# Kernel tuning notes

Hardware: AMD Instinct MI355X
Metric: run time of the kernel (lower is better)

The kernel has to match this reference:

```python
import jax, jax.numpy as jnp
import numpy as np
from jax import lax

B, C, D, H, W = 2, 1, 128, 128, 128
CONSCIOUSNESS_WEIGHT = 0.1


def _field(depth, height, width, dtype):
    # sin(2*pi*(d+h+w)/(D+H+W)) broadcast over batch/channel
    d = jnp.arange(depth, dtype=dtype)[:, None, None]
    h = jnp.arange(height, dtype=dtype)[None, :, None]
    w = jnp.arange(width, dtype=dtype)[None, None, :]
    phase = 2.0 * jnp.pi * (d + h + w) / (depth + height + width)
    return jnp.sin(phase)  # [D,H,W]


def _conv3d(x, w, b):
    y = lax.conv_general_dilated(
        x, w, window_strides=(1, 1, 1), padding='SAME',
        dimension_numbers=('NCDHW', 'OIDHW', 'NCDHW'))
    return y + b[None, :, None, None, None]


def setup_inputs() -> dict:
    key = jax.random.key(0)
    ks = jax.random.split(key, 4)
    fan1 = 1 * 27
    fan2 = 8 * 27
    fan3 = 16 * 27
    return {
        'cube_data': jax.random.normal(ks[0], (B, C, D, H, W), dtype=jnp.float32),
        'w1': jax.random.normal(ks[1], (8, 1, 3, 3, 3), dtype=jnp.float32) / np.sqrt(fan1),
        'b1': jnp.zeros((8,), dtype=jnp.float32),
        'w2': jax.random.normal(ks[2], (16, 8, 3, 3, 3), dtype=jnp.float32) / np.sqrt(fan2),
        'b2': jnp.zeros((16,), dtype=jnp.float32),
        'w3': jax.random.normal(ks[3], (1, 16, 3, 3, 3), dtype=jnp.float32) / np.sqrt(fan3),
        'b3': jnp.zeros((1,), dtype=jnp.float32),
    }


def reference(cube_data, w1, b1, w2, b2, w3, b3):
    _, _, d, h, w = cube_data.shape
    field = _field(d, h, w, cube_data.dtype)[None, None]  # [1,1,D,H,W]
    integrated = cube_data * (1.0 + CONSCIOUSNESS_WEIGHT * field)
    x = jax.nn.relu(_conv3d(integrated, w1, b1))
    x = jax.nn.relu(_conv3d(x, w2, b2))
    x = jnp.tanh(_conv3d(x, w3, b3))
    return x
```

## Files before the change

kernel.cpp:

```cpp
#include <hip/hip_runtime.h>
#include <hip/hip_fp16.h>

#define VOX (128 * 128 * 128)
#define P 130
#define PP (P * P)
#define PVOX (P * P * P)
#define LROW 130
#define PLANE (6 * LROW)

typedef unsigned short u16;
typedef _Float16 f16x2 __attribute__((ext_vector_type(2)));
typedef _Float16 f16x8 __attribute__((ext_vector_type(8)));
typedef __attribute__((ext_vector_type(4))) float f32x4;

__device__ __forceinline__ u16 f2h(float f) {
    return __builtin_bit_cast(unsigned short, (_Float16)f);
}
__device__ __forceinline__ unsigned pkh_relu(float a, float b) {
    float ra = a > 0.f ? a : 0.f, rb = b > 0.f ? b : 0.f;
    return (unsigned)f2h(ra) | ((unsigned)f2h(rb) << 16);
}
__device__ __forceinline__ f16x2 h2(unsigned u) { return __builtin_bit_cast(f16x2, u); }

__device__ __forceinline__ float dot2(unsigned a, unsigned b, float c) {
#if __has_builtin(__builtin_amdgcn_fdot2)
    return __builtin_amdgcn_fdot2(h2(a), h2(b), c, false);
#else
    f16x2 av = h2(a), bv = h2(b);
    c = fmaf((float)av.x, (float)bv.x, c);
    return fmaf((float)av.y, (float)bv.y, c);
#endif
}

__device__ __forceinline__ float fast_tanh(float x) {
    float e = __expf(2.0f * x);
    return 1.0f - 2.0f * __builtin_amdgcn_rcpf(1.0f + e);
}

__device__ __forceinline__ void gload_lds16(const u16* g, u16* l) {
    __builtin_amdgcn_global_load_lds(
        (const __attribute__((address_space(1))) unsigned int*)g,
        (__attribute__((address_space(3))) unsigned int*)l,
        16, 0, 0);
}

__global__ __launch_bounds__(256) void integrate_kernel(
    const float* __restrict__ in, u16* __restrict__ x0,
    const float* __restrict__ w1, const float* __restrict__ w2,
    const float* __restrict__ w3, u16* __restrict__ w2frag,
    unsigned* __restrict__ w3p, float* __restrict__ w1c,
    u16* __restrict__ x1, u16* __restrict__ x2) {
    int i = blockIdx.x * 256 + threadIdx.x;
    if (i < 3584) {
        int j = i & 7, l = (i >> 3) & 63, s = i >> 9;
        int tap = s * 4 + (l >> 4), oc = l & 15;
        float v = (tap < 27) ? w2[(oc * 8 + j) * 27 + tap] : 0.0f;
        w2frag[i] = f2h(v);
    }
    if (i < 216) {
        int tap = i >> 3, j = i & 7;
        w3p[i] = (unsigned)f2h(w3[(2 * j) * 27 + tap]) |
                 ((unsigned)f2h(w3[(2 * j + 1) * 27 + tap]) << 16);
        int c = i & 7;
        w1c[i] = w1[c * 27 + tap];
    }
    if (i >= PVOX) return;
    int d = i / PP;
    int r = i - d * PP;
    int h = r / P;
    int w = r - h * P;
    const bool interior = (d >= 1 && d <= 128 && h >= 1 && h <= 128 && w >= 1 && w <= 128);
    float v = 0.0f;
    if (interior) {
        int s = (d - 1) + (h - 1) + (w - 1);
        float fld = 1.0f + 0.1f * __sinf(6.283185307179586f * (float)s / 384.0f);
        v = in[(size_t)(d - 1) * 16384 + (h - 1) * 128 + (w - 1)] * fld;
    } else {
        uint4 z = {0u, 0u, 0u, 0u};
        *(uint4*)(x1 + (size_t)i * 8) = z;
        *(uint4*)(x2 + (size_t)i * 16) = z;
        *(uint4*)(x2 + (size_t)i * 16 + 8) = z;
    }
    x0[i] = f2h(v);
}

__global__ __launch_bounds__(256) void integrate_light_kernel(
    const float* __restrict__ in, u16* __restrict__ x0) {
    const int i = blockIdx.x * 256 + threadIdx.x;
    const int d = i >> 14, h = (i >> 7) & 127, w = i & 127;
    const int s = d + h + w;
    const float fld = 1.0f + 0.1f * __sinf((float)s * 0.016362461737446838f);
    x0[(size_t)(d + 1) * PP + (h + 1) * P + (w + 1)] = f2h(in[i] * fld);
}

__global__ __launch_bounds__(256) void conv1_kernel(
    const u16* __restrict__ x0, const float* __restrict__ w1c,
    const float* __restrict__ b1, u16* __restrict__ x1) {
    const int t = blockIdx.x * 256 + threadIdx.x;
    const int w0 = (t & 63) * 2;
    const int h0 = ((t >> 6) & 31) * 4;
    const int d = t >> 11;

    float acc[4][2][8];
#pragma unroll
    for (int c = 0; c < 8; ++c) {
        const float b = b1[c];
#pragma unroll
        for (int i = 0; i < 4; ++i) { acc[i][0][c] = b; acc[i][1][c] = b; }
    }

#pragma unroll
    for (int dz = 0; dz < 3; ++dz) {
        const u16* zb = x0 + (size_t)(d + dz) * PP + (size_t)h0 * P + w0;
        const float* wz = w1c + dz * 9 * 8;
#pragma unroll
        for (int r = 0; r < 6; ++r) {
            const u16* rp = zb + r * P;
            const unsigned u0 = *(const unsigned*)rp;
            const unsigned u1 = *(const unsigned*)(rp + 2);
            float vv[4];
            vv[0] = (float)h2(u0).x; vv[1] = (float)h2(u0).y;
            vv[2] = (float)h2(u1).x; vv[3] = (float)h2(u1).y;
#pragma unroll
            for (int dy = 0; dy < 3; ++dy) {
                const int i = r - dy;
                if (i < 0 || i > 3) continue;
#pragma unroll
                for (int dx = 0; dx < 3; ++dx) {
                    const float a0 = vv[dx];
                    const float a1 = vv[dx + 1];
                    const float* wp = wz + (dy * 3 + dx) * 8;
#pragma unroll
                    for (int c = 0; c < 8; ++c) {
                        const float wt = wp[c];
                        acc[i][0][c] = fmaf(wt, a0, acc[i][0][c]);
                        acc[i][1][c] = fmaf(wt, a1, acc[i][1][c]);
                    }
                }
            }
        }
    }
    const size_t e0 = ((size_t)(d + 1) * P + (h0 + 1)) * P + (w0 + 1);
#pragma unroll
    for (int i = 0; i < 4; ++i) {
        uint4 oA, oB;
        oA.x = pkh_relu(acc[i][0][0], acc[i][0][1]);
        oA.y = pkh_relu(acc[i][0][2], acc[i][0][3]);
        oA.z = pkh_relu(acc[i][0][4], acc[i][0][5]);
        oA.w = pkh_relu(acc[i][0][6], acc[i][0][7]);
        oB.x = pkh_relu(acc[i][1][0], acc[i][1][1]);
        oB.y = pkh_relu(acc[i][1][2], acc[i][1][3]);
        oB.z = pkh_relu(acc[i][1][4], acc[i][1][5]);
        oB.w = pkh_relu(acc[i][1][6], acc[i][1][7]);
        *(uint4*)(x1 + (e0 + (size_t)i * P) * 8) = oA;
        *(uint4*)(x1 + (e0 + (size_t)i * P + 1) * 8) = oB;
    }
}

__global__ __launch_bounds__(256) void conv2_mfma_kernel(
    const u16* __restrict__ x1, const u16* __restrict__ w2frag,
    const float* __restrict__ b2, u16* __restrict__ x2) {
    __shared__ u16 sm[4 * PLANE * 8];

    const int tid = threadIdx.x;
    const int lane = tid & 63;
    const int wv = tid >> 6;
    const int q = lane >> 4;
    const int mi = lane & 15;
    const int D0 = (blockIdx.x >> 5) * 8;
    const int h0 = (blockIdx.x & 31) * 4;

    f16x8 wf[7];
#pragma unroll
    for (int s = 0; s < 7; ++s)
        wf[s] = *(const f16x8*)(w2frag + (size_t)(s * 64 + lane) * 8);

#pragma unroll
    for (int p = 0; p < 3; ++p) {
        const int pd = D0 + p;
        const int slot = pd & 3;
        const u16* gb = x1 + ((size_t)(pd * P + h0) * P) * 8;
        u16* lb = sm + (size_t)slot * PLANE * 8;
#pragma unroll
        for (int k = 0; k < 3; ++k) {
            const int u0 = wv * 64 + k * 256;
            gload_lds16(gb + (size_t)(u0 + lane) * 8, lb + (size_t)u0 * 8);
        }
        if (wv == 0 && lane < PLANE - 768)
            gload_lds16(gb + (size_t)(768 + lane) * 8, lb + (size_t)768 * 8);
    }
    __syncthreads();

    const float4 bv = *(const float4*)(b2 + q * 4);

#pragma unroll 1
    for (int i = 0; i < 8; ++i) {
        const int dout = D0 + i;

        if (i < 7) {
            const int pd = dout + 3;
            const int slot = pd & 3;
            const u16* gb = x1 + ((size_t)(pd * P + h0) * P) * 8;
            u16* lb = sm + (size_t)slot * PLANE * 8;
#pragma unroll
            for (int k = 0; k < 3; ++k) {
                const int u0 = wv * 64 + k * 256;
                gload_lds16(gb + (size_t)(u0 + lane) * 8, lb + (size_t)u0 * 8);
            }
            if (wv == 0 && lane < PLANE - 768)
                gload_lds16(gb + (size_t)(768 + lane) * 8, lb + (size_t)768 * 8);
        }

        f32x4 acc[8];
#pragma unroll
        for (int t = 0; t < 8; ++t) acc[t] = (f32x4){0.f, 0.f, 0.f, 0.f};

#pragma unroll
        for (int s = 0; s < 7; ++s) {
            int tap = s * 4 + q;
            if (tap > 26) tap = 26;
            const int dz = tap / 9;
            const int rem = tap - dz * 9;
            const int dy = rem / 3;
            const int dx = rem - dy * 3;
            const int slot = (dout + dz) & 3;
            const u16* bp = sm + ((size_t)(slot * 6 + wv + dy) * LROW + (mi + dx)) * 8;
#pragma unroll
            for (int t = 0; t < 8; ++t) {
                f16x8 act = *(const f16x8*)(bp + t * 128);
                acc[t] = __builtin_amdgcn_mfma_f32_16x16x32_f16(wf[s], act, acc[t], 0, 0, 0);
            }
        }

        const size_t obase = ((size_t)(dout + 1) * P + (h0 + wv + 1)) * P + 1;
#pragma unroll
        for (int t = 0; t < 8; ++t) {
            uint2 o;
            o.x = pkh_relu(acc[t][0] + bv.x, acc[t][1] + bv.y);
            o.y = pkh_relu(acc[t][2] + bv.z, acc[t][3] + bv.w);
            *(uint2*)(x2 + (obase + 16 * t + mi) * 16 + q * 4) = o;
        }

        if (i < 7) __syncthreads();
    }
}

__global__ __launch_bounds__(256) void conv3_kernel(
    const u16* __restrict__ x2, const unsigned* __restrict__ w3p,
    const float* __restrict__ b3, float* __restrict__ out) {
    const int t = blockIdx.x * 256 + threadIdx.x;
    const int w0 = (t & 63) * 2;
    const int h0 = ((t >> 6) & 31) * 4;
    const int d0 = (t >> 11) * 2;

    float accA[2][4][2], accB[2][4][2];
#pragma unroll
    for (int dd = 0; dd < 2; ++dd)
#pragma unroll
        for (int i = 0; i < 4; ++i)
#pragma unroll
            for (int m = 0; m < 2; ++m) { accA[dd][i][m] = 0.f; accB[dd][i][m] = 0.f; }

#pragma unroll 1
    for (int z = 0; z < 4; ++z) {
        const u16* zb = x2 + ((size_t)((d0 + z) * P + h0) * P + w0) * 16;
#pragma unroll
        for (int r = 0; r < 6; ++r) {
            const u16* rp = zb + (size_t)r * (P * 16);
            uint4 v[8];
#pragma unroll
            for (int k = 0; k < 8; ++k) v[k] = *(const uint4*)(rp + k * 8);
#pragma unroll
            for (int dd = 0; dd < 2; ++dd) {
                const int dz = z - dd;
                if (dz < 0 || dz > 2) continue;
                const unsigned* wz = w3p + dz * 9 * 8;
#pragma unroll
                for (int dy = 0; dy < 3; ++dy) {
                    const int i = r - dy;
                    if (i < 0 || i > 3) continue;
                    const unsigned* wrow = wz + dy * 3 * 8;
#pragma unroll
                    for (int dx = 0; dx < 3; ++dx) {
                        const unsigned* wt = wrow + dx * 8;
#pragma unroll
                        for (int m = 0; m < 2; ++m) {
                            const uint4 lo = v[2 * (m + dx)];
                            const uint4 hi = v[2 * (m + dx) + 1];
                            float a = accA[dd][i][m], b = accB[dd][i][m];
                            a = dot2(lo.x, wt[0], a); b = dot2(lo.y, wt[1], b);
                            a = dot2(lo.z, wt[2], a); b = dot2(lo.w, wt[3], b);
                            a = dot2(hi.x, wt[4], a); b = dot2(hi.y, wt[5], b);
                            a = dot2(hi.z, wt[6], a); b = dot2(hi.w, wt[7], b);
                            accA[dd][i][m] = a; accB[dd][i][m] = b;
                        }
                    }
                }
            }
        }
    }
    const float bias = b3[0];
#pragma unroll
    for (int dd = 0; dd < 2; ++dd) {
#pragma unroll
        for (int i = 0; i < 4; ++i) {
            float2 o;
            o.x = fast_tanh(accA[dd][i][0] + accB[dd][i][0] + bias);
            o.y = fast_tanh(accA[dd][i][1] + accB[dd][i][1] + bias);
            *(float2*)(out + (size_t)((d0 + dd) * 128 + h0 + i) * 128 + w0) = o;
        }
    }
}

extern "C" void kernel_launch(void* const* d_in, const int* in_sizes, int n_in,
                              void* d_out, int out_size, void* d_ws, size_t ws_size,
                              hipStream_t stream) {
    const float* cube = (const float*)d_in[0];
    const float* w1 = (const float*)d_in[1];
    const float* b1 = (const float*)d_in[2];
    const float* w2 = (const float*)d_in[3];
    const float* b2 = (const float*)d_in[4];
    const float* w3 = (const float*)d_in[5];
    const float* b3 = (const float*)d_in[6];
    float* out = (float*)d_out;

    char* ws = (char*)d_ws;
    u16* w2frag = (u16*)ws;
    unsigned* w3p = (unsigned*)(ws + 7168);
    float* w1c = (float*)(ws + 8032);
    u16* x0 = (u16*)(ws + 16384);
    u16* x1 = (u16*)(ws + 16384 + (size_t)PVOX * sizeof(u16));
    u16* x2 = (u16*)(ws + 16384 + (size_t)PVOX * sizeof(u16) + (size_t)PVOX * 8 * sizeof(u16));

    for (int b = 0; b < 2; ++b) {
        if (b == 0) {
            integrate_kernel<<<dim3((PVOX + 255) / 256), dim3(256), 0, stream>>>(
                cube, x0, w1, w2, w3, w2frag, w3p, w1c, x1, x2);
        } else {
            integrate_light_kernel<<<dim3(VOX / 256), dim3(256), 0, stream>>>(
                cube + (size_t)VOX, x0);
        }
        conv1_kernel<<<dim3(VOX / 8 / 256), dim3(256), 0, stream>>>(x0, w1c, b1, x1);
        conv2_mfma_kernel<<<dim3(512), dim3(256), 0, stream>>>(x1, w2frag, b2, x2);
        conv3_kernel<<<dim3(VOX / 16 / 256), dim3(256), 0, stream>>>(
            x2, w3p, b3, out + (size_t)b * VOX);
    }
}
```

Before: 219.0 us.

## Restructure conv3 to stream depth planes through LDS with rolling buffer

The final 16→1 channel conv now stages haloed x2 slabs into a four-slot LDS ring using direct global-to-LDS loads, and each block walks eight output depth planes over a four-row band. The next plane is prefetched while the current one is computed. Weights are held in registers, and each pair of threads splits the 16 channels and combines its partial sums with a lane shuffle. This aims to cut redundant global reads of overlapping neighbourhoods. In exchange it adds barriers, heavy register use at one block per CU, and less work per thread.

```diff
diff --git a/kernel.cpp b/kernel.cpp
--- a/kernel.cpp
+++ b/kernel.cpp
@@ -7,6 +7,7 @@
 #define PVOX (P * P * P)
 #define LROW 130
 #define PLANE (6 * LROW)
+#define C3PLANE 1560
 
 typedef unsigned short u16;
 typedef _Float16 f16x2 __attribute__((ext_vector_type(2)));
@@ -245,70 +246,101 @@
     }
 }
 
-__global__ __launch_bounds__(256) void conv3_kernel(
+__global__ __launch_bounds__(256, 1) void conv3_kernel(
     const u16* __restrict__ x2, const unsigned* __restrict__ w3p,
     const float* __restrict__ b3, float* __restrict__ out) {
-    const int t = blockIdx.x * 256 + threadIdx.x;
-    const int w0 = (t & 63) * 2;
-    const int h0 = ((t >> 6) & 31) * 4;
-    const int d0 = (t >> 11) * 2;
-
-    float accA[2][4][2], accB[2][4][2];
-#pragma unroll
-    for (int dd = 0; dd < 2; ++dd)
-#pragma unroll
-        for (int i = 0; i < 4; ++i)
-#pragma unroll
-            for (int m = 0; m < 2; ++m) { accA[dd][i][m] = 0.f; accB[dd][i][m] = 0.f; }
+    __shared__ u16 sm[4 * C3PLANE * 8];
+
+    const int tid = threadIdx.x;
+    const int lane = tid & 63;
+    const int wv = tid >> 6;
+    const int half = tid & 1;
+    const int p = tid >> 1;
+    const int D0 = (blockIdx.x >> 5) * 8;
+    const int h0 = (blockIdx.x & 31) * 4;
+
+    uint4 wt[27];
+#pragma unroll
+    for (int q = 0; q < 27; ++q)
+        wt[q] = *(const uint4*)(w3p + q * 8 + half * 4);
+
+#pragma unroll
+    for (int pp = 0; pp < 3; ++pp) {
+        const int pd = D0 + pp;
+        const int slot = pd & 3;
+        const u16* gb = x2 + ((size_t)(pd * P + h0) * P) * 16;
+        u16* lb = sm + (size_t)slot * C3PLANE * 8;
+#pragma unroll
+        for (int k = 0; k < 6; ++k) {
+            const int u0 = wv * 64 + k * 256;
+            gload_lds16(gb + (size_t)(u0 + lane) * 8, lb + (size_t)u0 * 8);
+        }
+        if (wv == 0 && lane < C3PLANE - 1536)
+            gload_lds16(gb + (size_t)(1536 + lane) * 8, lb + (size_t)1536 * 8);
+    }
+    __syncthreads();
+
+    const float bias = b3[0];
 
 #pragma unroll 1
-    for (int z = 0; z < 4; ++z) {
-        const u16* zb = x2 + ((size_t)((d0 + z) * P + h0) * P + w0) * 16;
-#pragma unroll
-        for (int r = 0; r < 6; ++r) {
-            const u16* rp = zb + (size_t)r * (P * 16);
-            uint4 v[8];
-#pragma unroll
-            for (int k = 0; k < 8; ++k) v[k] = *(const uint4*)(rp + k * 8);
-#pragma unroll
-            for (int dd = 0; dd < 2; ++dd) {
-                const int dz = z - dd;
-                if (dz < 0 || dz > 2) continue;
-                const unsigned* wz = w3p + dz * 9 * 8;
+    for (int i = 0; i < 8; ++i) {
+        const int dout = D0 + i;
+
+        if (i < 7) {
+            const int pd = dout + 3;
+            const int slot = pd & 3;
+            const u16* gb = x2 + ((size_t)(pd * P + h0) * P) * 16;
+            u16* lb = sm + (size_t)slot * C3PLANE * 8;
+#pragma unroll
+            for (int k = 0; k < 6; ++k) {
+                const int u0 = wv * 64 + k * 256;
+                gload_lds16(gb + (size_t)(u0 + lane) * 8, lb + (size_t)u0 * 8);
+            }
+            if (wv == 0 && lane < C3PLANE - 1536)
+                gload_lds16(gb + (size_t)(1536 + lane) * 8, lb + (size_t)1536 * 8);
+        }
+
+        float acc[4] = {0.f, 0.f, 0.f, 0.f};
+#pragma unroll
+        for (int dz = 0; dz < 3; ++dz) {
+            const int slot = (dout + dz) & 3;
+            const u16* sp = sm + (size_t)slot * C3PLANE * 8 + (size_t)half * 8;
+#pragma unroll
+            for (int r = 0; r < 6; ++r) {
+                const u16* rp = sp + (size_t)(r * 130 + p) * 16;
+                const uint4 v0 = *(const uint4*)(rp);
+                const uint4 v1 = *(const uint4*)(rp + 16);
+                const uint4 v2 = *(const uint4*)(rp + 32);
 #pragma unroll
                 for (int dy = 0; dy < 3; ++dy) {
-                    const int i = r - dy;
-                    if (i < 0 || i > 3) continue;
-                    const unsigned* wrow = wz + dy * 3 * 8;
+                    const int ii = r - dy;
+                    if (ii < 0 || ii > 3) continue;
 #pragma unroll
                     for (int dx = 0; dx < 3; ++dx) {
-                        const unsigned* wt = wrow + dx * 8;
-#pragma unroll
-                        for (int m = 0; m < 2; ++m) {
-                            const uint4 lo = v[2 * (m + dx)];
-                            const uint4 hi = v[2 * (m + dx) + 1];
-                            float a = accA[dd][i][m], b = accB[dd][i][m];
-                            a = dot2(lo.x, wt[0], a); b = dot2(lo.y, wt[1], b);
-                            a = dot2(lo.z, wt[2], a); b = dot2(lo.w, wt[3], b);
-                            a = dot2(hi.x, wt[4], a); b = dot2(hi.y, wt[5], b);
-                            a = dot2(hi.z, wt[6], a); b = dot2(hi.w, wt[7], b);
-                            accA[dd][i][m] = a; accB[dd][i][m] = b;
-                        }
+                        const uint4 wq = wt[dz * 9 + dy * 3 + dx];
+                        const uint4 v = (dx == 0) ? v0 : ((dx == 1) ? v1 : v2);
+                        float a = acc[ii];
+                        a = dot2(v.x, wq.x, a);
+                        a = dot2(v.y, wq.y, a);
+                        a = dot2(v.z, wq.z, a);
+                        a = dot2(v.w, wq.w, a);
+                        acc[ii] = a;
                     }
                 }
             }
         }
-    }
-    const float bias = b3[0];
-#pragma unroll
-    for (int dd = 0; dd < 2; ++dd) {
-#pragma unroll
-        for (int i = 0; i < 4; ++i) {
-            float2 o;
-            o.x = fast_tanh(accA[dd][i][0] + accB[dd][i][0] + bias);
-            o.y = fast_tanh(accA[dd][i][1] + accB[dd][i][1] + bias);
-            *(float2*)(out + (size_t)((d0 + dd) * 128 + h0 + i) * 128 + w0) = o;
-        }
+
+#pragma unroll
+        for (int k = 0; k < 4; ++k) acc[k] += __shfl_xor(acc[k], 1);
+
+        const size_t ob = ((size_t)dout * 128 + h0) * 128 + p;
+#pragma unroll
+        for (int k = 0; k < 2; ++k) {
+            const int hr = half * 2 + k;
+            out[ob + (size_t)hr * 128] = fast_tanh(acc[hr] + bias);
+        }
+
+        if (i < 7) __syncthreads();
     }
 }
 
@@ -342,7 +374,7 @@
         }
         conv1_kernel<<<dim3(VOX / 8 / 256), dim3(256), 0, stream>>>(x0, w1c, b1, x1);
         conv2_mfma_kernel<<<dim3(512), dim3(256), 0, stream>>>(x1, w2frag, b2, x2);
-        conv3_kernel<<<dim3(VOX / 16 / 256), dim3(256), 0, stream>>>(
+        conv3_kernel<<<dim3(512), dim3(256), 0, stream>>>(
             x2, w3p, b3, out + (size_t)b * VOX);
     }
 }
```

Result: slower. 234.9 us (+7.3%).
